# Performance work log

Measured on AMD Instinct MI355X. Metric: run time of the kernel, lower is better.

## Reference

```python
import jax, jax.numpy as jnp
import numpy as np

E = 1024      # embed_dim
H = 16        # num_heads
HD = E // H   # head_dim = 64
M = 64        # num_landmarks


def setup_inputs() -> dict:
    key = jax.random.key(0)
    ks = jax.random.split(key, 9)
    B, Lq, Lk = 2, 2048, 2048
    inv = 1.0 / np.sqrt(E)
    return {
        "query": jax.random.normal(ks[0], (B, Lq, E), dtype=jnp.float32),
        "key":   jax.random.normal(ks[1], (B, Lk, E), dtype=jnp.float32),
        "value": jax.random.normal(ks[2], (B, Lk, E), dtype=jnp.float32),
        # learned params (xavier-ish scale)
        "Wv": jax.random.normal(ks[3], (E, E), dtype=jnp.float32) * inv,
        "bv": jnp.zeros((E,), dtype=jnp.float32),
        "Wl": jax.random.normal(ks[4], (M, E), dtype=jnp.float32) * inv,
        "bl": jnp.zeros((M,), dtype=jnp.float32),
        "Wo": jax.random.normal(ks[5], (E, E), dtype=jnp.float32) * inv,
        "bo": jnp.zeros((E,), dtype=jnp.float32),
    }


def reference(query, key, value, Wv, bv, Wl, bl, Wo, bo):
    B, Lq, _ = query.shape
    Lk = key.shape[1]
    # value projection -> [B, H, Lk, HD]
    v = (value @ Wv.T + bv).reshape(B, Lk, H, HD).transpose(0, 2, 1, 3)
    # landmark projections + softmax over landmark dim
    ql = jax.nn.softmax((query @ Wl.T + bl) / np.sqrt(M), axis=-1)  # [B, Lq, M]
    kl = jax.nn.softmax((key @ Wl.T + bl) / np.sqrt(M), axis=-1)    # [B, Lk, M]
    # landmark attention: [B, Lq, Lk], scaled by sqrt(head_dim), softmax over keys
    attn = jax.nn.softmax(
        jnp.einsum("bqm,bkm->bqk", ql, kl) / np.sqrt(HD), axis=-1)
    # apply shared attention across heads: [B, H, Lq, HD]
    out_h = jnp.einsum("bqk,bhkd->bhqd", attn, v)
    out = out_h.transpose(0, 2, 1, 3).reshape(B, Lq, E)
    return out @ Wo.T + bo
```

## Files before the change

kernel.cpp:

```cpp
#include <hip/hip_runtime.h>
#include <hip/hip_bf16.h>
#include <cstdint>

typedef unsigned short u16;
typedef __attribute__((ext_vector_type(8))) short short8;
typedef __attribute__((ext_vector_type(4))) float f32x4;
typedef __attribute__((ext_vector_type(4))) unsigned short us4;

__device__ __forceinline__ u16 f2bf(float f) {
    union { float f; unsigned int i; } v; v.f = f;
    unsigned int x = v.i;
    unsigned int r = x + 0x7fffu + ((x >> 16) & 1u);
    return (u16)(r >> 16);
}

enum { EPI_F32 = 0, EPI_BF16 = 1, EPI_EXP_RS = 3, EPI_F32_DIV_CB = 4, EPI_LMSM = 5 };

template <int BM, int BN, int EPI, bool AF32, bool BF32>
__global__ void __launch_bounds__(256)
gemm_bt(const void* __restrict__ Ax, const void* __restrict__ A2x,
        const void* __restrict__ Bx, void* __restrict__ Cv,
        int M, int N, int K, long sA, long sB, long sC,
        const float* __restrict__ biasCol, float* __restrict__ rowScale, float expScale)
{
    constexpr int BK = 64;
    constexpr int MFRAG = (BM + 31) / 32;
    constexpr int NFRAG = BN / 32;
    constexpr int AG = (BM + 31) / 32;
    constexpr int BG = BN / 32;
    __shared__ alignas(16) u16 As[BM * BK];
    __shared__ alignas(16) u16 Bs[BN * BK];

    const int tid = threadIdx.x;
    const int lane = tid & 63;
    const int quad = lane >> 4;
    const int l15 = lane & 15;
    const int w = tid >> 6;
    const int wm = w >> 1, wn = w & 1;
    const int z = blockIdx.z;
    const int m0 = blockIdx.y * BM;
    const int n0 = blockIdx.x * BN;

    const int r8 = tid >> 3;
    const int cl = tid & 7;
    const int cg = ((cl ^ (r8 & 7)) * 8);

    const u16* ap[AG];
    const float* apf[AG];
    if constexpr (AF32) {
        const float* base = (const float*)Ax;
        long mr = m0;
        if (A2x != nullptr && m0 >= (M >> 1)) { base = (const float*)A2x; mr = m0 - (M >> 1); }
        const float* Afb = base + (long)z * sA + (long)mr * K;
#pragma unroll
        for (int j = 0; j < AG; ++j) apf[j] = Afb + (long)(j * 32 + r8) * K + cg;
    } else {
        const u16* Ab = (const u16*)Ax + (long)z * sA + (long)m0 * K;
#pragma unroll
        for (int j = 0; j < AG; ++j) ap[j] = Ab + (long)(j * 32 + r8) * K + cg;
    }
    const u16* bp[BG];
    const float* bpf[BG];
    if constexpr (BF32) {
        const float* Bfb = (const float*)Bx + (long)z * sB + (long)n0 * K;
#pragma unroll
        for (int j = 0; j < BG; ++j) bpf[j] = Bfb + (long)(j * 32 + r8) * K + cg;
    } else {
        const u16* Bb = (const u16*)Bx + (long)z * sB + (long)n0 * K;
#pragma unroll
        for (int j = 0; j < BG; ++j) bp[j] = Bb + (long)(j * 32 + r8) * K + cg;
    }

    f32x4 acc[MFRAG][NFRAG] = {};

    const int sw = l15 & 7;

    for (int k0 = 0; k0 < K; k0 += BK) {
        if constexpr (!AF32) {
#pragma unroll
            for (int j = 0; j < AG; ++j) {
                __builtin_amdgcn_global_load_lds(
                    (const __attribute__((address_space(1))) void*)(ap[j]),
                    (__attribute__((address_space(3))) void*)(&As[(j * 32 + r8) * BK + cl * 8]),
                    16, 0, 0);
                ap[j] += BK;
            }
        }
        if constexpr (!BF32) {
#pragma unroll
            for (int j = 0; j < BG; ++j) {
                __builtin_amdgcn_global_load_lds(
                    (const __attribute__((address_space(1))) void*)(bp[j]),
                    (__attribute__((address_space(3))) void*)(&Bs[(j * 32 + r8) * BK + cl * 8]),
                    16, 0, 0);
                bp[j] += BK;
            }
        }
        if constexpr (AF32) {
#pragma unroll
            for (int j = 0; j < AG; ++j) {
                const float4 u0 = *(const float4*)(apf[j]);
                const float4 u1 = *(const float4*)(apf[j] + 4);
                short8 o;
                o[0] = (short)f2bf(u0.x); o[1] = (short)f2bf(u0.y);
                o[2] = (short)f2bf(u0.z); o[3] = (short)f2bf(u0.w);
                o[4] = (short)f2bf(u1.x); o[5] = (short)f2bf(u1.y);
                o[6] = (short)f2bf(u1.z); o[7] = (short)f2bf(u1.w);
                *(short8*)&As[(j * 32 + r8) * BK + cl * 8] = o;
                apf[j] += BK;
            }
        }
        if constexpr (BF32) {
#pragma unroll
            for (int j = 0; j < BG; ++j) {
                const float4 u0 = *(const float4*)(bpf[j]);
                const float4 u1 = *(const float4*)(bpf[j] + 4);
                short8 o;
                o[0] = (short)f2bf(u0.x); o[1] = (short)f2bf(u0.y);
                o[2] = (short)f2bf(u0.z); o[3] = (short)f2bf(u0.w);
                o[4] = (short)f2bf(u1.x); o[5] = (short)f2bf(u1.y);
                o[6] = (short)f2bf(u1.z); o[7] = (short)f2bf(u1.w);
                *(short8*)&Bs[(j * 32 + r8) * BK + cl * 8] = o;
                bpf[j] += BK;
            }
        }
        __syncthreads();
#pragma unroll
        for (int ks = 0; ks < 2; ++ks) {
            short8 af[MFRAG], bfr[NFRAG];
#pragma unroll
            for (int i = 0; i < MFRAG; ++i)
                af[i] = *(const short8*)&As[(wm * (BM / 2) + i * 16 + l15) * BK +
                                            (((ks * 4 + quad) ^ sw) * 8)];
#pragma unroll
            for (int i = 0; i < NFRAG; ++i)
                bfr[i] = *(const short8*)&Bs[(wn * (BN / 2) + i * 16 + l15) * BK +
                                             (((ks * 4 + quad) ^ sw) * 8)];
#pragma unroll
            for (int i = 0; i < MFRAG; ++i)
#pragma unroll
                for (int jn = 0; jn < NFRAG; ++jn)
                    acc[i][jn] = __builtin_amdgcn_mfma_f32_16x16x32_bf16(af[i], bfr[jn], acc[i][jn], 0, 0, 0);
        }
        __syncthreads();
    }

    if constexpr (EPI == EPI_LMSM) {
        __shared__ float red[2][BM];
        float ev[4][NFRAG];
#pragma unroll
        for (int r = 0; r < 4; ++r) {
            float s = 0.f;
#pragma unroll
            for (int jn = 0; jn < NFRAG; ++jn) {
                const int col = wn * (BN / 2) + jn * 16 + l15;
                float v = exp2f((acc[0][jn][r] + biasCol[col]) * expScale);
                ev[r][jn] = v; s += v;
            }
            s += __shfl_xor(s, 1); s += __shfl_xor(s, 2);
            s += __shfl_xor(s, 4); s += __shfl_xor(s, 8);
            if (l15 == 0) red[wn][wm * 16 + quad * 4 + r] = s;
        }
        __syncthreads();
#pragma unroll
        for (int r = 0; r < 4; ++r) {
            const int mrow = wm * 16 + quad * 4 + r;
            const float inv = 1.0f / (red[0][mrow] + red[1][mrow]);
            const long m = m0 + mrow;
#pragma unroll
            for (int jn = 0; jn < NFRAG; ++jn) {
                const int col = wn * (BN / 2) + jn * 16 + l15;
                ((u16*)Cv)[m * N + col] = f2bf(ev[r][jn] * inv);
            }
        }
        return;
    } else {
#pragma unroll
        for (int i = 0; i < MFRAG; ++i) {
            const int mb = m0 + wm * (BM / 2) + i * 16 + quad * 4;
#pragma unroll
            for (int r = 0; r < 4; ++r) {
                const int m = mb + r;
                float rin = 0.f;
                if constexpr (EPI == EPI_F32_DIV_CB) rin = 1.0f / rowScale[(long)z * M + m];
                float rowsum = 0.f;
#pragma unroll
                for (int jn = 0; jn < NFRAG; ++jn) {
                    const int col = n0 + wn * (BN / 2) + jn * 16 + l15;
                    float v = acc[i][jn][r];
                    if constexpr (EPI == EPI_EXP_RS) { v = exp2f(v * expScale); rowsum += v; }
                    if constexpr (EPI == EPI_F32_DIV_CB) v = v * rin + biasCol[col];
                    if constexpr (EPI == EPI_F32 || EPI == EPI_F32_DIV_CB)
                        ((float*)Cv)[(long)z * sC + (long)m * N + col] = v;
                    else
                        ((u16*)Cv)[(long)z * sC + (long)m * N + col] = f2bf(v);
                }
                if constexpr (EPI == EPI_EXP_RS) {
                    rowsum += __shfl_xor(rowsum, 1);
                    rowsum += __shfl_xor(rowsum, 2);
                    rowsum += __shfl_xor(rowsum, 4);
                    rowsum += __shfl_xor(rowsum, 8);
                    if (l15 == 0) atomicAdd(&rowScale[(long)z * M + m], rowsum);
                }
            }
        }
    }
}

__global__ void __launch_bounds__(256)
prep_all(const float* __restrict__ Wo, const float* __restrict__ Wl,
         const float* __restrict__ Wv, const float* __restrict__ bv,
         const float* __restrict__ bo,
         u16* __restrict__ Wob, u16* __restrict__ Wlb, u16* __restrict__ WvT,
         float* __restrict__ rsc, float* __restrict__ bocomb)
{
    __shared__ float t[64][65];
    const int b = blockIdx.x;
    const int tid = threadIdx.x;
    if (b < 1088) {
        long i = ((long)b * 256 + tid) * 4;
        const float* s; u16* d;
        if (i < 1048576) { s = Wo; d = Wob; }
        else { i -= 1048576; s = Wl; d = Wlb; }
        const float4 v = *(const float4*)(s + i);
        us4 o;
        o.x = f2bf(v.x); o.y = f2bf(v.y); o.z = f2bf(v.z); o.w = f2bf(v.w);
        *(us4*)(d + i) = o;
    } else if (b < 1344) {
        const int bidx = b - 1088;
        const int bx = bidx & 15, by = bidx >> 4;
#pragma unroll
        for (int p = 0; p < 16; ++p) {
            int idx = p * 256 + tid;
            int r = idx >> 6, c = idx & 63;
            t[r][c] = Wv[(long)(by * 64 + r) * 1024 + bx * 64 + c];
        }
        __syncthreads();
#pragma unroll
        for (int p = 0; p < 16; ++p) {
            int idx = p * 256 + tid;
            int c = idx >> 6, r = idx & 63;
            WvT[(long)(bx * 64 + c) * 1024 + by * 64 + r] = f2bf(t[r][c]);
        }
        if (bx == 0) rsc[by * 256 + tid] = 0.f;
    } else {
        const int row = (b - 1344) * 4 + (tid >> 6);
        const int lane = tid & 63;
        float s = 0.f;
#pragma unroll
        for (int i = 0; i < 16; ++i) s += Wo[(long)row * 1024 + i * 64 + lane] * bv[i * 64 + lane];
        for (int o = 32; o; o >>= 1) s += __shfl_xor(s, o, 64);
        if (lane == 0) bocomb[row] = bo[row] + s;
    }
}

extern "C" void kernel_launch(void* const* d_in, const int* in_sizes, int n_in,
                              void* d_out, int out_size, void* d_ws, size_t ws_size,
                              hipStream_t stream)
{
    const float* query = (const float*)d_in[0];
    const float* key   = (const float*)d_in[1];
    const float* value = (const float*)d_in[2];
    const float* Wv    = (const float*)d_in[3];
    const float* bv    = (const float*)d_in[4];
    const float* Wl    = (const float*)d_in[5];
    const float* bl    = (const float*)d_in[6];
    const float* Wo    = (const float*)d_in[7];
    const float* bo    = (const float*)d_in[8];
    float* out = (float*)d_out;

    char* ws = (char*)d_ws;
    u16*   Wlb    = (u16*)  (ws + 25165824);
    u16*   Wob    = (u16*)  (ws + 25296896);
    u16*   WvT    = (u16*)  (ws + 27394048);
    u16*   Wov    = (u16*)  (ws + 29491200);
    u16*   qlkl   = (u16*)  (ws + 31588352);
    u16*   Ut     = (u16*)  (ws + 32636928);
    u16*   Pm     = (u16*)  (ws + 41025536);
    float* rsc    = (float*)(ws + 57802752);
    float* bocomb = (float*)(ws + 57819136);

    prep_all<<<dim3(1600), 256, 0, stream>>>(Wo, Wl, Wv, bv, bo,
                                             Wob, Wlb, WvT, rsc, bocomb);

    gemm_bt<32, 64, EPI_LMSM, true, false><<<dim3(1, 256, 1), 256, 0, stream>>>(
        query, key, Wlb, qlkl, 8192, 64, 1024, 0, 0, 0, bl, nullptr, 0.18033688011112042f);

    gemm_bt<64, 64, EPI_BF16, false, false><<<dim3(16, 16, 1), 256, 0, stream>>>(
        Wob, nullptr, WvT, Wov, 1024, 1024, 1024, 0, 0, 0, nullptr, nullptr, 0.f);

    gemm_bt<128, 64, EPI_BF16, false, true><<<dim3(32, 8, 2), 256, 0, stream>>>(
        Wov, nullptr, value, Ut, 1024, 2048, 1024, 0, 2097152, 2097152, nullptr, nullptr, 0.f);

    gemm_bt<128, 128, EPI_EXP_RS, false, false><<<dim3(16, 16, 2), 256, 0, stream>>>(
        qlkl, nullptr, qlkl + 262144, Pm, 2048, 2048, 64,
        131072, 131072, 4194304, nullptr, rsc, 0.18033688011112042f);

    gemm_bt<64, 128, EPI_F32_DIV_CB, false, false><<<dim3(8, 32, 2), 256, 0, stream>>>(
        Pm, nullptr, Ut, out, 2048, 1024, 2048,
        4194304, 2097152, 2097152, bocomb, rsc, 0.f);
}
```

Before: 194.4 us.

## Merge independent GEMMs into shared launches and convert Wo inside GEMM

Turns the GEMM into a device body that works on dynamic shared memory, then merges independent GEMMs into single launches: the landmark projection with the Wo·Wv product, and the value projection with the landmark score GEMM. The Wo bf16 conversion pass is removed from prep, and Wo is read as fp32 and converted directly in the GEMM. This cuts the launch count from six to four and drops a weight conversion round trip. In exchange the merged kernels have divergent block types with different tile shapes, which can unbalance occupancy and scheduling.

Measured after the change: 178.0 us. 1.09x faster.

```diff
diff --git a/kernel.cpp b/kernel.cpp
--- a/kernel.cpp
+++ b/kernel.cpp
@@ -17,19 +17,21 @@
 enum { EPI_F32 = 0, EPI_BF16 = 1, EPI_EXP_RS = 3, EPI_F32_DIV_CB = 4, EPI_LMSM = 5 };
 
 template <int BM, int BN, int EPI, bool AF32, bool BF32>
-__global__ void __launch_bounds__(256)
-gemm_bt(const void* __restrict__ Ax, const void* __restrict__ A2x,
-        const void* __restrict__ Bx, void* __restrict__ Cv,
-        int M, int N, int K, long sA, long sB, long sC,
-        const float* __restrict__ biasCol, float* __restrict__ rowScale, float expScale)
+__device__ __forceinline__ void gemm_body(
+    char* __restrict__ smem,
+    const void* __restrict__ Ax, const void* __restrict__ A2x,
+    const void* __restrict__ Bx, void* __restrict__ Cv,
+    int M, int N, int K, long sA, long sB, long sC,
+    const float* __restrict__ biasCol, float* __restrict__ rowScale, float expScale,
+    int m0, int n0, int z)
 {
     constexpr int BK = 64;
     constexpr int MFRAG = (BM + 31) / 32;
     constexpr int NFRAG = BN / 32;
     constexpr int AG = (BM + 31) / 32;
     constexpr int BG = BN / 32;
-    __shared__ alignas(16) u16 As[BM * BK];
-    __shared__ alignas(16) u16 Bs[BN * BK];
+    u16* As = (u16*)smem;
+    u16* Bs = (u16*)(smem + (long)BM * BK * 2);
 
     const int tid = threadIdx.x;
     const int lane = tid & 63;
@@ -37,9 +39,6 @@
     const int l15 = lane & 15;
     const int w = tid >> 6;
     const int wm = w >> 1, wn = w & 1;
-    const int z = blockIdx.z;
-    const int m0 = blockIdx.y * BM;
-    const int n0 = blockIdx.x * BN;
 
     const int r8 = tid >> 3;
     const int cl = tid & 7;
@@ -146,7 +145,7 @@
     }
 
     if constexpr (EPI == EPI_LMSM) {
-        __shared__ float red[2][BM];
+        float* red = (float*)(smem + (long)(BM + BN) * BK * 2);
         float ev[4][NFRAG];
 #pragma unroll
         for (int r = 0; r < 4; ++r) {
@@ -159,13 +158,13 @@
             }
             s += __shfl_xor(s, 1); s += __shfl_xor(s, 2);
             s += __shfl_xor(s, 4); s += __shfl_xor(s, 8);
-            if (l15 == 0) red[wn][wm * 16 + quad * 4 + r] = s;
+            if (l15 == 0) red[wn * BM + wm * 16 + quad * 4 + r] = s;
         }
         __syncthreads();
 #pragma unroll
         for (int r = 0; r < 4; ++r) {
             const int mrow = wm * 16 + quad * 4 + r;
-            const float inv = 1.0f / (red[0][mrow] + red[1][mrow]);
+            const float inv = 1.0f / (red[mrow] + red[BM + mrow]);
             const long m = m0 + mrow;
 #pragma unroll
             for (int jn = 0; jn < NFRAG; ++jn) {
@@ -207,27 +206,77 @@
     }
 }
 
+template <int BM, int BN, int EPI, bool AF32, bool BF32>
 __global__ void __launch_bounds__(256)
-prep_all(const float* __restrict__ Wo, const float* __restrict__ Wl,
-         const float* __restrict__ Wv, const float* __restrict__ bv,
+gemm_bt(const void* __restrict__ Ax, const void* __restrict__ A2x,
+        const void* __restrict__ Bx, void* __restrict__ Cv,
+        int M, int N, int K, long sA, long sB, long sC,
+        const float* __restrict__ biasCol, float* __restrict__ rowScale, float expScale)
+{
+    extern __shared__ char smem[];
+    gemm_body<BM, BN, EPI, AF32, BF32>(smem, Ax, A2x, Bx, Cv, M, N, K, sA, sB, sC,
+                                       biasCol, rowScale, expScale,
+                                       blockIdx.y * BM, blockIdx.x * BN, blockIdx.z);
+}
+
+__global__ void __launch_bounds__(256)
+fused23(const float* __restrict__ query, const float* __restrict__ key,
+        const u16* __restrict__ Wlb, u16* __restrict__ qlkl,
+        const float* __restrict__ bl,
+        const float* __restrict__ Wo, const u16* __restrict__ WvT, u16* __restrict__ Wov)
+{
+    extern __shared__ char smem[];
+    const int b = blockIdx.x;
+    if (b < 256) {
+        gemm_body<32, 64, EPI_LMSM, true, false>(smem, query, key, Wlb, qlkl,
+            8192, 64, 1024, 0, 0, 0, bl, nullptr, 0.18033688011112042f,
+            b * 32, 0, 0);
+    } else {
+        const int t = b - 256;
+        gemm_body<64, 64, EPI_BF16, true, false>(smem, Wo, nullptr, WvT, Wov,
+            1024, 1024, 1024, 0, 0, 0, nullptr, nullptr, 0.f,
+            (t >> 4) * 64, (t & 15) * 64, 0);
+    }
+}
+
+__global__ void __launch_bounds__(256)
+fused45(const u16* __restrict__ Wov, const float* __restrict__ value, u16* __restrict__ Ut,
+        const u16* __restrict__ qlkl, u16* __restrict__ Pm, float* __restrict__ rsc)
+{
+    extern __shared__ char smem[];
+    const int b = blockIdx.x;
+    if (b < 512) {
+        const int x = b & 31, y = (b >> 5) & 7, z = b >> 8;
+        gemm_body<128, 64, EPI_BF16, false, true>(smem, Wov, nullptr, value, Ut,
+            1024, 2048, 1024, 0, 2097152, 2097152, nullptr, nullptr, 0.f,
+            y * 128, x * 64, z);
+    } else {
+        const int t = b - 512;
+        const int x = t & 15, y = (t >> 4) & 15, z = t >> 8;
+        gemm_body<128, 128, EPI_EXP_RS, false, false>(smem, qlkl, nullptr, qlkl + 262144, Pm,
+            2048, 2048, 64, 131072, 131072, 4194304, nullptr, rsc, 0.18033688011112042f,
+            y * 128, x * 128, z);
+    }
+}
+
+__global__ void __launch_bounds__(256)
+prep_all(const float* __restrict__ Wl, const float* __restrict__ Wv,
+         const float* __restrict__ Wo, const float* __restrict__ bv,
          const float* __restrict__ bo,
-         u16* __restrict__ Wob, u16* __restrict__ Wlb, u16* __restrict__ WvT,
+         u16* __restrict__ Wlb, u16* __restrict__ WvT,
          float* __restrict__ rsc, float* __restrict__ bocomb)
 {
     __shared__ float t[64][65];
     const int b = blockIdx.x;
     const int tid = threadIdx.x;
-    if (b < 1088) {
+    if (b < 64) {
         long i = ((long)b * 256 + tid) * 4;
-        const float* s; u16* d;
-        if (i < 1048576) { s = Wo; d = Wob; }
-        else { i -= 1048576; s = Wl; d = Wlb; }
-        const float4 v = *(const float4*)(s + i);
+        const float4 v = *(const float4*)(Wl + i);
         us4 o;
         o.x = f2bf(v.x); o.y = f2bf(v.y); o.z = f2bf(v.z); o.w = f2bf(v.w);
-        *(us4*)(d + i) = o;
-    } else if (b < 1344) {
-        const int bidx = b - 1088;
+        *(us4*)(Wlb + i) = o;
+    } else if (b < 320) {
+        const int bidx = b - 64;
         const int bx = bidx & 15, by = bidx >> 4;
 #pragma unroll
         for (int p = 0; p < 16; ++p) {
@@ -244,7 +293,7 @@
         }
         if (bx == 0) rsc[by * 256 + tid] = 0.f;
     } else {
-        const int row = (b - 1344) * 4 + (tid >> 6);
+        const int row = (b - 320) * 4 + (tid >> 6);
         const int lane = tid & 63;
         float s = 0.f;
 #pragma unroll
@@ -271,7 +320,6 @@
 
     char* ws = (char*)d_ws;
     u16*   Wlb    = (u16*)  (ws + 25165824);
-    u16*   Wob    = (u16*)  (ws + 25296896);
     u16*   WvT    = (u16*)  (ws + 27394048);
     u16*   Wov    = (u16*)  (ws + 29491200);
     u16*   qlkl   = (u16*)  (ws + 31588352);
@@ -280,23 +328,16 @@
     float* rsc    = (float*)(ws + 57802752);
     float* bocomb = (float*)(ws + 57819136);
 
-    prep_all<<<dim3(1600), 256, 0, stream>>>(Wo, Wl, Wv, bv, bo,
-                                             Wob, Wlb, WvT, rsc, bocomb);
-
-    gemm_bt<32, 64, EPI_LMSM, true, false><<<dim3(1, 256, 1), 256, 0, stream>>>(
-        query, key, Wlb, qlkl, 8192, 64, 1024, 0, 0, 0, bl, nullptr, 0.18033688011112042f);
-
-    gemm_bt<64, 64, EPI_BF16, false, false><<<dim3(16, 16, 1), 256, 0, stream>>>(
-        Wob, nullptr, WvT, Wov, 1024, 1024, 1024, 0, 0, 0, nullptr, nullptr, 0.f);
-
-    gemm_bt<128, 64, EPI_BF16, false, true><<<dim3(32, 8, 2), 256, 0, stream>>>(
-        Wov, nullptr, value, Ut, 1024, 2048, 1024, 0, 2097152, 2097152, nullptr, nullptr, 0.f);
-
-    gemm_bt<128, 128, EPI_EXP_RS, false, false><<<dim3(16, 16, 2), 256, 0, stream>>>(
-        qlkl, nullptr, qlkl + 262144, Pm, 2048, 2048, 64,
-        131072, 131072, 4194304, nullptr, rsc, 0.18033688011112042f);
-
-    gemm_bt<64, 128, EPI_F32_DIV_CB, false, false><<<dim3(8, 32, 2), 256, 0, stream>>>(
+    prep_all<<<dim3(576), 256, 0, stream>>>(Wl, Wv, Wo, bv, bo,
+                                            Wlb, WvT, rsc, bocomb);
+
+    fused23<<<dim3(512), 256, 16384, stream>>>(query, key, Wlb, qlkl, bl,
+                                               Wo, WvT, Wov);
+
+    fused45<<<dim3(1024), 256, 32768, stream>>>(Wov, value, Ut, qlkl, Pm, rsc);
+
+    gemm_bt<64, 128, EPI_F32_DIV_CB, false, false>
+        <<<dim3(8, 32, 2), 256, 24576, stream>>>(
         Pm, nullptr, Ut, out, 2048, 1024, 2048,
         4194304, 2097152, 2097152, bocomb, rsc, 0.f);
 }
```
